# Kernel tuning notes

Hardware: AMD Instinct MI355X
Metric: run time of the kernel (lower is better)

## Reference

```python
import jax, jax.numpy as jnp
import numpy as np

B, N, F, H = 1024, 64, 128, 8

def _xavier(k, shape):
    fan_in, fan_out = shape
    lim = (6.0 / (fan_in + fan_out)) ** 0.5
    return jax.random.uniform(k, shape, jnp.float32, -lim, lim)

def setup_inputs() -> dict:
    key = jax.random.key(0)
    ks = jax.random.split(key, 7)
    return {
        "x": jax.random.normal(ks[0], (B, N, F), jnp.float32),
        # zeroth-order MLP params
        "Wz0": _xavier(ks[1], (F, H)), "bz0": jnp.zeros((H,), jnp.float32),
        "Wz1": _xavier(ks[2], (H, H)), "bz1": jnp.zeros((H,), jnp.float32),
        "wsz": _xavier(ks[3], (H, 1)), "bsz": jnp.zeros((1,), jnp.float32),
        # first-order (pairwise) MLP params; Wf0 takes cat(x_i, x_j) of width 2F
        "Wf0": _xavier(ks[4], (2 * F, H)), "bf0": jnp.zeros((H,), jnp.float32),
        "Wf1": _xavier(ks[5], (H, H)), "bf1": jnp.zeros((H,), jnp.float32),
        # scorer_first takes cat(f(i,j), f(j,i)) of width 2H
        "wsf": _xavier(ks[6], (2 * H, 1)), "bsf": jnp.zeros((1,), jnp.float32),
    }

def reference(x, Wz0, bz0, Wz1, bz1, wsz, bsz, Wf0, bf0, Wf1, bf1, wsf, bsf):
    selu = jax.nn.selu
    n = x.shape[1]
    f_dim = x.shape[-1]
    h_dim = Wf1.shape[0]

    # ---- zeroth-order scores: per-object MLP, vectorized over (B, N) ----
    h = selu(x @ Wz0 + bz0)
    h = selu(h @ Wz1 + bz1)
    zeroth = selu(h @ wsz + bsz)[..., 0]  # [B, N]

    # ---- first-order: batched over all ordered pairs (i, j), i != j ----
    # cat(x_i, x_j) @ Wf0 == x_i @ Wf0[:F] + x_j @ Wf0[F:]  (avoids [B,N,N,2F] concat)
    Wa, Wb = Wf0[:f_dim], Wf0[f_dim:]
    hi = x @ Wa  # [B, N, H]
    hj = x @ Wb  # [B, N, H]
    f = selu(hi[:, :, None, :] + hj[:, None, :, :] + bf0)  # [B, N, N, H] = hidden of pair (i, j)
    f = selu(f @ Wf1 + bf1)

    # scorer_first on cat(f(i,j), f(j,i)): split weight into left/right halves
    wl, wr = wsf[:h_dim], wsf[h_dim:]
    S = (f @ wl + jnp.swapaxes(f, 1, 2) @ wr)[..., 0] + bsf[0]  # [B, N, N]; S[b,i,j] = score_left of (i,j)

    # outputs[i] collects S[b,i,j] for all j != i; mean over the n-1 partners
    mask = 1.0 - jnp.eye(n, dtype=S.dtype)
    pair_mean = (S * mask).sum(axis=2) / (n - 1)  # [B, N]

    return pair_mean + zeroth
```

## Files before the change

kernel.cpp:

```cpp
#include <hip/hip_runtime.h>


#define SELU_ALPHA 1.6732632423543772f
#define SELU_SCALE 1.0507009873554805f

__device__ __forceinline__ float selu_f(float x) {
    float neg = fmaf(SELU_ALPHA, __expf(x), -SELU_ALPHA);
    return SELU_SCALE * (x > 0.0f ? x : neg);
}

__global__ __launch_bounds__(128) void feta_k1(
    const float* __restrict__ x,
    const float* __restrict__ Wz0, const float* __restrict__ bz0,
    const float* __restrict__ Wz1, const float* __restrict__ bz1,
    const float* __restrict__ wsz, const float* __restrict__ bsz,
    const float* __restrict__ Wf0, const float* __restrict__ bf0,
    float* __restrict__ hi_out, float* __restrict__ hj_out,
    float* __restrict__ z_out)
{
    __shared__ float xs[128 * 129];
    __shared__ float w0[128 * 8];
    __shared__ float wa[128 * 8];
    __shared__ float wb[128 * 8];

    const int t = threadIdx.x;
    const long long rowbase = (long long)blockIdx.x * 128;

    const float4* xin = (const float4*)(x + rowbase * 128);
    #pragma unroll
    for (int it = 0; it < 32; ++it) {
        int f4 = it * 128 + t;
        float4 v = xin[f4];
        int flat = f4 * 4;
        int r = flat >> 7;
        int c = flat & 127;
        float* dst = &xs[r * 129 + c];
        dst[0] = v.x; dst[1] = v.y; dst[2] = v.z; dst[3] = v.w;
    }
    for (int idx = t; idx < 1024; idx += 128) {
        w0[idx] = Wz0[idx];
        wa[idx] = Wf0[idx];
        wb[idx] = Wf0[1024 + idx];
    }
    __syncthreads();

    float az[8], aa[8], ab[8];
    #pragma unroll
    for (int c = 0; c < 8; ++c) { az[c] = bz0[c]; aa[c] = 0.f; ab[c] = 0.f; }

    const float* myrow = &xs[t * 129];
    for (int k = 0; k < 128; ++k) {
        float xk = myrow[k];
        #pragma unroll
        for (int c = 0; c < 8; ++c) {
            az[c] = fmaf(xk, w0[k * 8 + c], az[c]);
            aa[c] = fmaf(xk, wa[k * 8 + c], aa[c]);
            ab[c] = fmaf(xk, wb[k * 8 + c], ab[c]);
        }
    }

    const long long gr = rowbase + t;
    float* hip = hi_out + gr * 8;
    float* hjp = hj_out + gr * 8;
    #pragma unroll
    for (int c = 0; c < 8; ++c) {
        hip[c] = aa[c] + bf0[c];
        hjp[c] = ab[c];
    }

    float h0[8];
    #pragma unroll
    for (int c = 0; c < 8; ++c) h0[c] = selu_f(az[c]);
    float zacc = bsz[0];
    #pragma unroll
    for (int c = 0; c < 8; ++c) {
        float s = bz1[c];
        #pragma unroll
        for (int r = 0; r < 8; ++r) s = fmaf(h0[r], Wz1[r * 8 + c], s);
        zacc = fmaf(selu_f(s), wsz[c], zacc);
    }
    z_out[gr] = selu_f(zacc);
}

__global__ __launch_bounds__(256) void feta_k2(
    const float* __restrict__ hi, const float* __restrict__ hj,
    const float* __restrict__ z,
    const float* __restrict__ Wf1, const float* __restrict__ bf1,
    const float* __restrict__ wsf, const float* __restrict__ bsf,
    float* __restrict__ out)
{
    __shared__ float his[64 * 8];
    __shared__ float ts[64 * 65];
    __shared__ float cup[4 * 64];
    __shared__ float rsp[4 * 64];

    const int b = blockIdx.x;
    const int t = threadIdx.x;
    const int w = t >> 6;
    const int l = t & 63;
    const long long base = (long long)b * 64 * 8;

    if (t < 128) ((float4*)his)[t] = ((const float4*)(hi + base))[t];

    float hjr[8];
    {
        const float4* hp = (const float4*)(hj + base + l * 8);
        float4 v0 = hp[0], v1 = hp[1];
        hjr[0] = v0.x; hjr[1] = v0.y; hjr[2] = v0.z; hjr[3] = v0.w;
        hjr[4] = v1.x; hjr[5] = v1.y; hjr[6] = v1.z; hjr[7] = v1.w;
    }

    float W[64], bf[8], wl[8], wr[8];
    #pragma unroll
    for (int i = 0; i < 64; ++i) W[i] = Wf1[i];
    #pragma unroll
    for (int c = 0; c < 8; ++c) { bf[c] = bf1[c]; wl[c] = wsf[c]; wr[c] = wsf[8 + c]; }
    const float bsfv = bsf[0];
    __syncthreads();

    float cu_acc = 0.f;
    for (int k = 0; k < 16; ++k) {
        const int i = w * 16 + k;
        const float* hrow = &his[i * 8];
        float g[8];
        #pragma unroll
        for (int c = 0; c < 8; ++c) g[c] = selu_f(hrow[c] + hjr[c]);
        float tt = 0.f, uu = 0.f;
        #pragma unroll
        for (int c = 0; c < 8; ++c) {
            float s = bf[c];
            #pragma unroll
            for (int r = 0; r < 8; ++r) s = fmaf(g[r], W[r * 8 + c], s);
            float fv = selu_f(s);
            tt = fmaf(fv, wl[c], tt);
            uu = fmaf(fv, wr[c], uu);
        }
        if (i == l) { tt = 0.f; uu = 0.f; }
        cu_acc += uu;
        ts[i * 65 + l] = tt;
    }
    cup[w * 64 + l] = cu_acc;
    __syncthreads();

    float rp = 0.f;
    #pragma unroll
    for (int m = 0; m < 16; ++m) rp += ts[l * 65 + w * 16 + m];
    rsp[w * 64 + l] = rp;
    __syncthreads();

    if (t < 64) {
        float rsum = rsp[t] + rsp[64 + t] + rsp[128 + t] + rsp[192 + t];
        float csum = cup[t] + cup[64 + t] + cup[128 + t] + cup[192 + t];
        out[(long long)b * 64 + t] =
            (rsum + csum) * (1.0f / 63.0f) + bsfv + z[(long long)b * 64 + t];
    }
}

extern "C" void kernel_launch(void* const* d_in, const int* in_sizes, int n_in,
                              void* d_out, int out_size, void* d_ws, size_t ws_size,
                              hipStream_t stream) {
    const float* x   = (const float*)d_in[0];
    const float* Wz0 = (const float*)d_in[1];
    const float* bz0 = (const float*)d_in[2];
    const float* Wz1 = (const float*)d_in[3];
    const float* bz1 = (const float*)d_in[4];
    const float* wsz = (const float*)d_in[5];
    const float* bsz = (const float*)d_in[6];
    const float* Wf0 = (const float*)d_in[7];
    const float* bf0 = (const float*)d_in[8];
    const float* Wf1 = (const float*)d_in[9];
    const float* bf1 = (const float*)d_in[10];
    const float* wsf = (const float*)d_in[11];
    const float* bsf = (const float*)d_in[12];
    float* out = (float*)d_out;

    float* hi_ws = (float*)d_ws;
    float* hj_ws = hi_ws + 65536 * 8;
    float* z_ws  = hj_ws + 65536 * 8;

    feta_k1<<<512, 128, 0, stream>>>(x, Wz0, bz0, Wz1, bz1, wsz, bsz,
                                     Wf0, bf0, hi_ws, hj_ws, z_ws);
    feta_k2<<<1024, 256, 0, stream>>>(hi_ws, hj_ws, z_ws, Wf1, bf1, wsf, bsf, out);
}
```

Before: 132.2 us.

## Fuse projection and pairwise kernels into one per-batch kernel

Merges the two kernels into one block per batch. Each block loads x into shared memory and splits the zeroth-order MLP, the hi projection and the hj projection across its wavefronts, then runs the pairwise stage on shared-memory results. This removes the workspace round trip for hi/hj/z and one launch, and folds the SELU scale into Wf1 and wsf. In exchange the per-object projection now reads weights from global/constant memory instead of shared, and wave-level work in the first phase is imbalanced.

```diff
diff --git a/kernel.cpp b/kernel.cpp
--- a/kernel.cpp
+++ b/kernel.cpp
@@ -4,134 +4,133 @@
 #define SELU_ALPHA 1.6732632423543772f
 #define SELU_SCALE 1.0507009873554805f
 
-__device__ __forceinline__ float selu_f(float x) {
+__device__ __forceinline__ float selu_full(float x) {
     float neg = fmaf(SELU_ALPHA, __expf(x), -SELU_ALPHA);
     return SELU_SCALE * (x > 0.0f ? x : neg);
 }
+__device__ __forceinline__ float sel_unscaled(float x) {
+    float neg = fmaf(SELU_ALPHA, __expf(x), -SELU_ALPHA);
+    return x > 0.0f ? x : neg;
+}
 
-__global__ __launch_bounds__(128) void feta_k1(
+__global__ __launch_bounds__(256) void feta_fused(
     const float* __restrict__ x,
     const float* __restrict__ Wz0, const float* __restrict__ bz0,
     const float* __restrict__ Wz1, const float* __restrict__ bz1,
     const float* __restrict__ wsz, const float* __restrict__ bsz,
     const float* __restrict__ Wf0, const float* __restrict__ bf0,
-    float* __restrict__ hi_out, float* __restrict__ hj_out,
-    float* __restrict__ z_out)
-{
-    __shared__ float xs[128 * 129];
-    __shared__ float w0[128 * 8];
-    __shared__ float wa[128 * 8];
-    __shared__ float wb[128 * 8];
-
-    const int t = threadIdx.x;
-    const long long rowbase = (long long)blockIdx.x * 128;
-
-    const float4* xin = (const float4*)(x + rowbase * 128);
-    #pragma unroll
-    for (int it = 0; it < 32; ++it) {
-        int f4 = it * 128 + t;
-        float4 v = xin[f4];
-        int flat = f4 * 4;
-        int r = flat >> 7;
-        int c = flat & 127;
-        float* dst = &xs[r * 129 + c];
-        dst[0] = v.x; dst[1] = v.y; dst[2] = v.z; dst[3] = v.w;
-    }
-    for (int idx = t; idx < 1024; idx += 128) {
-        w0[idx] = Wz0[idx];
-        wa[idx] = Wf0[idx];
-        wb[idx] = Wf0[1024 + idx];
-    }
-    __syncthreads();
-
-    float az[8], aa[8], ab[8];
-    #pragma unroll
-    for (int c = 0; c < 8; ++c) { az[c] = bz0[c]; aa[c] = 0.f; ab[c] = 0.f; }
-
-    const float* myrow = &xs[t * 129];
-    for (int k = 0; k < 128; ++k) {
-        float xk = myrow[k];
-        #pragma unroll
-        for (int c = 0; c < 8; ++c) {
-            az[c] = fmaf(xk, w0[k * 8 + c], az[c]);
-            aa[c] = fmaf(xk, wa[k * 8 + c], aa[c]);
-            ab[c] = fmaf(xk, wb[k * 8 + c], ab[c]);
-        }
-    }
-
-    const long long gr = rowbase + t;
-    float* hip = hi_out + gr * 8;
-    float* hjp = hj_out + gr * 8;
-    #pragma unroll
-    for (int c = 0; c < 8; ++c) {
-        hip[c] = aa[c] + bf0[c];
-        hjp[c] = ab[c];
-    }
-
-    float h0[8];
-    #pragma unroll
-    for (int c = 0; c < 8; ++c) h0[c] = selu_f(az[c]);
-    float zacc = bsz[0];
-    #pragma unroll
-    for (int c = 0; c < 8; ++c) {
-        float s = bz1[c];
-        #pragma unroll
-        for (int r = 0; r < 8; ++r) s = fmaf(h0[r], Wz1[r * 8 + c], s);
-        zacc = fmaf(selu_f(s), wsz[c], zacc);
-    }
-    z_out[gr] = selu_f(zacc);
-}
-
-__global__ __launch_bounds__(256) void feta_k2(
-    const float* __restrict__ hi, const float* __restrict__ hj,
-    const float* __restrict__ z,
     const float* __restrict__ Wf1, const float* __restrict__ bf1,
     const float* __restrict__ wsf, const float* __restrict__ bsf,
     float* __restrict__ out)
 {
-    __shared__ float his[64 * 8];
-    __shared__ float ts[64 * 65];
-    __shared__ float cup[4 * 64];
-    __shared__ float rsp[4 * 64];
+    __shared__ float smem[64 * 129];
+    __shared__ float his[64 * 12];
+    __shared__ float hjs[64 * 12];
+    __shared__ float zs[64];
 
     const int b = blockIdx.x;
     const int t = threadIdx.x;
     const int w = t >> 6;
     const int l = t & 63;
-    const long long base = (long long)b * 64 * 8;
 
-    if (t < 128) ((float4*)his)[t] = ((const float4*)(hi + base))[t];
+    {
+        const float4* xin = (const float4*)(x + (long long)b * 8192);
+        #pragma unroll
+        for (int i = 0; i < 8; ++i) {
+            int f4 = i * 256 + t;
+            float4 v = xin[f4];
+            int r  = f4 >> 5;
+            int kq = f4 & 31;
+            *(float4*)&smem[r * 129 + kq * 4] = v;
+        }
+    }
+    __syncthreads();
+
+    const float* xr = &smem[l * 129];
+    if (w == 0) {
+        float acc[8];
+        #pragma unroll
+        for (int c = 0; c < 8; ++c) acc[c] = bz0[c];
+        #pragma unroll 8
+        for (int k = 0; k < 128; ++k) {
+            float xk = xr[k];
+            #pragma unroll
+            for (int c = 0; c < 8; ++c) acc[c] = fmaf(xk, Wz0[k * 8 + c], acc[c]);
+        }
+        float h0[8];
+        #pragma unroll
+        for (int c = 0; c < 8; ++c) h0[c] = selu_full(acc[c]);
+        float zacc = bsz[0];
+        #pragma unroll
+        for (int c = 0; c < 8; ++c) {
+            float s = bz1[c];
+            #pragma unroll
+            for (int r = 0; r < 8; ++r) s = fmaf(h0[r], Wz1[r * 8 + c], s);
+            zacc = fmaf(selu_full(s), wsz[c], zacc);
+        }
+        zs[l] = selu_full(zacc);
+    } else if (w == 1) {
+        float acc[8];
+        #pragma unroll
+        for (int c = 0; c < 8; ++c) acc[c] = bf0[c];
+        #pragma unroll 8
+        for (int k = 0; k < 128; ++k) {
+            float xk = xr[k];
+            #pragma unroll
+            for (int c = 0; c < 8; ++c) acc[c] = fmaf(xk, Wf0[k * 8 + c], acc[c]);
+        }
+        #pragma unroll
+        for (int c = 0; c < 8; ++c) his[l * 12 + c] = acc[c];
+    } else {
+        const int c0 = (w == 3) ? 4 : 0;
+        const float* wb = Wf0 + 1024 + c0;
+        float acc[4];
+        #pragma unroll
+        for (int c = 0; c < 4; ++c) acc[c] = 0.f;
+        #pragma unroll 8
+        for (int k = 0; k < 128; ++k) {
+            float xk = xr[k];
+            #pragma unroll
+            for (int c = 0; c < 4; ++c) acc[c] = fmaf(xk, wb[k * 8 + c], acc[c]);
+        }
+        #pragma unroll
+        for (int c = 0; c < 4; ++c) hjs[l * 12 + c0 + c] = acc[c];
+    }
+
+    float W[64], bfv[8], wl[8], wr[8];
+    #pragma unroll
+    for (int i = 0; i < 64; ++i) W[i] = SELU_SCALE * Wf1[i];
+    #pragma unroll
+    for (int c = 0; c < 8; ++c) {
+        bfv[c] = bf1[c];
+        wl[c]  = SELU_SCALE * wsf[c];
+        wr[c]  = SELU_SCALE * wsf[8 + c];
+    }
+    const float bsfv = bsf[0];
+    __syncthreads();
 
     float hjr[8];
-    {
-        const float4* hp = (const float4*)(hj + base + l * 8);
-        float4 v0 = hp[0], v1 = hp[1];
-        hjr[0] = v0.x; hjr[1] = v0.y; hjr[2] = v0.z; hjr[3] = v0.w;
-        hjr[4] = v1.x; hjr[5] = v1.y; hjr[6] = v1.z; hjr[7] = v1.w;
-    }
+    #pragma unroll
+    for (int c = 0; c < 8; ++c) hjr[c] = hjs[l * 12 + c];
 
-    float W[64], bf[8], wl[8], wr[8];
-    #pragma unroll
-    for (int i = 0; i < 64; ++i) W[i] = Wf1[i];
-    #pragma unroll
-    for (int c = 0; c < 8; ++c) { bf[c] = bf1[c]; wl[c] = wsf[c]; wr[c] = wsf[8 + c]; }
-    const float bsfv = bsf[0];
-    __syncthreads();
+    float* ts  = smem;
+    float* cup = smem + 64 * 65;
+    float* rsp = cup + 256;
 
     float cu_acc = 0.f;
     for (int k = 0; k < 16; ++k) {
         const int i = w * 16 + k;
-        const float* hrow = &his[i * 8];
+        const float* hrow = &his[i * 12];
         float g[8];
         #pragma unroll
-        for (int c = 0; c < 8; ++c) g[c] = selu_f(hrow[c] + hjr[c]);
+        for (int c = 0; c < 8; ++c) g[c] = sel_unscaled(hrow[c] + hjr[c]);
         float tt = 0.f, uu = 0.f;
         #pragma unroll
         for (int c = 0; c < 8; ++c) {
-            float s = bf[c];
+            float s = bfv[c];
             #pragma unroll
             for (int r = 0; r < 8; ++r) s = fmaf(g[r], W[r * 8 + c], s);
-            float fv = selu_f(s);
+            float fv = sel_unscaled(s);
             tt = fmaf(fv, wl[c], tt);
             uu = fmaf(fv, wr[c], uu);
         }
@@ -152,7 +151,7 @@
         float rsum = rsp[t] + rsp[64 + t] + rsp[128 + t] + rsp[192 + t];
         float csum = cup[t] + cup[64 + t] + cup[128 + t] + cup[192 + t];
         out[(long long)b * 64 + t] =
-            (rsum + csum) * (1.0f / 63.0f) + bsfv + z[(long long)b * 64 + t];
+            (rsum + csum) * (1.0f / 63.0f) + bsfv + zs[t];
     }
 }
 
@@ -174,11 +173,6 @@
     const float* bsf = (const float*)d_in[12];
     float* out = (float*)d_out;
 
-    float* hi_ws = (float*)d_ws;
-    float* hj_ws = hi_ws + 65536 * 8;
-    float* z_ws  = hj_ws + 65536 * 8;
-
-    feta_k1<<<512, 128, 0, stream>>>(x, Wz0, bz0, Wz1, bz1, wsz, bsz,
-                                     Wf0, bf0, hi_ws, hj_ws, z_ws);
-    feta_k2<<<1024, 256, 0, stream>>>(hi_ws, hj_ws, z_ws, Wf1, bf1, wsf, bsf, out);
+    feta_fused<<<1024, 256, 0, stream>>>(x, Wz0, bz0, Wz1, bz1, wsz, bsz,
+                                         Wf0, bf0, Wf1, bf1, wsf, bsf, out);
 }
```

Result: faster. 118.2 us (-10.6%).
